# Performance work log

Hardware: AMD Instinct MI355X
Metric: run time of the kernel (lower is better)

The kernel has to match this reference:

```python
import jax, jax.numpy as jnp
import numpy as np

T, B, E, H = 2048, 2, 1024, 16
S = E // H


def setup_inputs() -> dict:
    key = jax.random.key(0)
    ks = jax.random.split(key, 7)
    sc = 1.0 / np.sqrt(S)
    return {
        "x": jax.random.normal(ks[0], (T, B, E), dtype=jnp.float32),
        "Wq": jax.random.normal(ks[1], (H, S, S), dtype=jnp.float32) * sc,
        "Wk": jax.random.normal(ks[2], (H, S, S), dtype=jnp.float32) * sc,
        "Wv": jax.random.normal(ks[3], (H, S, S), dtype=jnp.float32) * sc,
        "Er": jax.random.normal(ks[4], (S, T), dtype=jnp.float32),
        "Wr": jax.random.normal(ks[5], (E, E), dtype=jnp.float32) * (1.0 / np.sqrt(E)),
        "br": jax.random.normal(ks[6], (E,), dtype=jnp.float32) * 0.01,
    }


def reference(x, Wq, Wk, Wv, Er, Wr, br):
    # x: [t, b, e] -> [b, t, h, s]
    t, b, e = x.shape
    h = Wq.shape[0]
    s = e // h
    xh = jnp.transpose(x, (1, 0, 2)).reshape(b, t, h, s)
    # per-head no-bias linears (nn.Linear: y = x @ W.T), stacked over heads
    q = jnp.einsum('bths,hds->bhtd', xh, Wq)  # [b,h,t,s]
    k = jnp.einsum('bths,hds->bhtd', xh, Wk)
    v = jnp.einsum('bths,hds->bhtd', xh, Wv)
    # relative bias uses UNSCALED queries (computed before the 1/e^(1/4) scaling)
    srel = jnp.einsum('bhtd,dr->bhtr', q, Er)  # [b,h,t,t] since r == t
    scale = e ** 0.25
    scores = jnp.einsum('bhtd,bhrd->bhtr', q / scale, k / scale) + srel
    causal = jnp.triu(jnp.ones((t, t), dtype=bool), 1)
    scores = jnp.where(causal[None, None], jnp.float32(-1e9), scores)
    probs = jax.nn.softmax(scores, axis=-1)  # dropout is identity in eval
    out = jnp.einsum('bhtr,bhrd->bhtd', probs, v)  # [b,h,t,s]
    # torch.cat(heads, dim=2) == move head axis next to s
    out = jnp.transpose(out, (0, 2, 1, 3)).reshape(b, t, h * s)  # [b,t,e]
    # faithful to source quirk: transpose(1,2).contiguous().view(b,t,e)
    out = jnp.swapaxes(out, 1, 2).reshape(b, t, h * s)
    return out @ Wr.T + br
```

## Files before the change

kernel.cpp:

```cpp
#include <hip/hip_runtime.h>
#include <hip/hip_bf16.h>
#include <cstdio>

#define T_DIM 2048
#define B_DIM 2
#define E_DIM 1024
#define H_DIM 16
#define S_DIM 64
#define LOG2E 1.44269504088896340736f

typedef __attribute__((ext_vector_type(4))) float f32x4;
typedef __attribute__((ext_vector_type(16))) float f32x16;
typedef __attribute__((ext_vector_type(8))) short bf16x8;
typedef __attribute__((ext_vector_type(8))) unsigned short u16x8;
typedef __attribute__((ext_vector_type(4))) unsigned short u16x4;

#define MFMA32(a,b,c) __builtin_amdgcn_mfma_f32_32x32x16_bf16((a),(b),(c),0,0,0)

__device__ __forceinline__ unsigned short f2bf(float f) {
    union { __hip_bfloat16 h; unsigned short u; } c;
    c.h = __float2bfloat16(f);
    return c.u;
}
__device__ __forceinline__ void gload16(const void* g, void* l) {
    __builtin_amdgcn_global_load_lds(
        (const __attribute__((address_space(1))) unsigned int*)g,
        (__attribute__((address_space(3))) unsigned int*)l, 16, 0, 0);
}
__device__ __forceinline__ f32x16 zero16() {
    f32x16 v;
#pragma unroll
    for (int i = 0; i < 16; ++i) v[i] = 0.f;
    return v;
}

__global__ __launch_bounds__(256) void prep_w(
    const float* __restrict__ Wq, const float* __restrict__ Wk,
    const float* __restrict__ Wv, const float* __restrict__ Wr,
    unsigned short* __restrict__ whb, unsigned short* __restrict__ wrb)
{
    int bid = blockIdx.x;
    if (bid < 192) {
        int i = bid * 256 + threadIdx.x;
        const float* src = (i < 16384) ? Wq : ((i < 32768) ? Wk : Wv);
        float4 v = reinterpret_cast<const float4*>(src)[i & 16383];
        u16x4 o;
        o[0] = f2bf(v.x); o[1] = f2bf(v.y); o[2] = f2bf(v.z); o[3] = f2bf(v.w);
        *reinterpret_cast<u16x4*>(whb + (size_t)i * 4) = o;
    } else {
        int i = (bid - 192) * 256 + threadIdx.x;
        float4 v = reinterpret_cast<const float4*>(Wr)[i];
        u16x4 o;
        o[0] = f2bf(v.x); o[1] = f2bf(v.y); o[2] = f2bf(v.z); o[3] = f2bf(v.w);
        *reinterpret_cast<u16x4*>(wrb + (size_t)i * 4) = o;
    }
}

__global__ __launch_bounds__(64) void qkv_mfma(
    const float* __restrict__ x, const unsigned short* __restrict__ wb,
    const float* __restrict__ Er,
    unsigned short* __restrict__ qb_g, unsigned short* __restrict__ kh_g,
    unsigned short* __restrict__ vT_g)
{
    int bid = blockIdx.x;
    int dg = bid & 1;
    int tt = (bid >> 1) & 63;
    int h  = (bid >> 7) & 15;
    int b  = bid >> 11;
    int bh = b * H_DIM + h;
    int t0 = tt * 32;
    int lane = threadIdx.x;
    int l31 = lane & 31, hs = lane >> 5;

    bf16x8 xb[4];
    const float* xrow = x + (size_t)(t0 + l31) * (B_DIM * E_DIM) + (size_t)b * E_DIM + h * 64;
#pragma unroll
    for (int ks = 0; ks < 4; ++ks) {
        float vv[8];
        *reinterpret_cast<float4*>(&vv[0]) = *reinterpret_cast<const float4*>(xrow + ks * 16 + hs * 8);
        *reinterpret_cast<float4*>(&vv[4]) = *reinterpret_cast<const float4*>(xrow + ks * 16 + hs * 8 + 4);
        unsigned short hh[8];
#pragma unroll
        for (int j = 0; j < 8; ++j) hh[j] = f2bf(vv[j]);
        xb[ks] = *reinterpret_cast<bf16x8*>(hh);
    }

    f32x16 aq = zero16(), ak = zero16(), av = zero16();
    size_t wofs = (size_t)h * 4096 + (size_t)(dg * 32 + l31) * 64 + hs * 8;
#pragma unroll
    for (int ks = 0; ks < 4; ++ks) {
        bf16x8 qw = *reinterpret_cast<const bf16x8*>(wb + wofs + ks * 16);
        bf16x8 kw = *reinterpret_cast<const bf16x8*>(wb + 65536 + wofs + ks * 16);
        bf16x8 vw = *reinterpret_cast<const bf16x8*>(wb + 131072 + wofs + ks * 16);
        aq = MFMA32(xb[ks], qw, aq);
        ak = MFMA32(xb[ks], kw, ak);
        av = MFMA32(vw, xb[ks], av);
    }

    size_t rowbase = (size_t)bh * T_DIM * 64;
#pragma unroll
    for (int r = 0; r < 16; ++r) {
        int rowp = (r & 3) + 8 * (r >> 2) + 4 * hs;
        int t = t0 + rowp;
        int d = dg * 32 + l31;
        size_t ro = rowbase + (size_t)t * 64 + d;
        qb_g[ro] = f2bf(aq[r]);
        float kv = (ak[r] * 0.03125f + Er[(size_t)d * T_DIM + t]) * LOG2E;
        kh_g[ro] = f2bf(kv);
        vT_g[((size_t)bh * 64 + dg * 32 + rowp) * T_DIM + t0 + l31] = f2bf(av[r]);
    }
}

__global__ __launch_bounds__(256, 4) void attn_mfma32(
    const unsigned short* __restrict__ qb_g, const unsigned short* __restrict__ kh_g,
    const unsigned short* __restrict__ vT_g, unsigned short* __restrict__ attT)
{
    __shared__ __align__(16) unsigned char smem[33024];
    float* OT  = (float*)smem;
    float* MRG = (float*)smem;
    float* ML  = (float*)(smem + 32768);

    int bid = blockIdx.x;
    int bh = bid & 31;
    int u = bid >> 5;
    int j = u & 7, quad = u >> 3;
    int qt = (quad == 0) ? (31 - j) : (quad == 1) ? j
           : (quad == 2) ? (23 - j) : (8 + j);

    int tid = threadIdx.x;
    int w = tid >> 6;
    int half = w >> 1;
    int wq = w & 1;
    int lane = tid & 63;
    int l31 = lane & 31, hs = lane >> 5;
    int srow = lane >> 3, scol = lane & 7;
    int q_lo = qt * 64 + wq * 32;
    size_t base = (size_t)bh * T_DIM * 64;

    bf16x8 qB[4];
    {
        size_t qoff = base + (size_t)(q_lo + l31) * 64 + hs * 8;
#pragma unroll
        for (int st = 0; st < 4; ++st)
            qB[st] = *reinterpret_cast<const bf16x8*>(qb_g + qoff + st * 16);
    }

    f32x16 oacc0 = zero16(), oacc1 = zero16();
    float lsum = 0.f;

    unsigned char* KH = smem + half * 16384;
    unsigned char* VT = KH + 8192;

    int ntiles = qt + 1;
    int nst = (ntiles + 1) >> 1;

    for (int i = 0; i < nst; ++i) {
        int k0 = (2 * i + half) * 64;
        bool valid = k0 < ntiles * 64;
        __syncthreads();
        if (valid) {
#pragma unroll
            for (int ci = 0; ci < 4; ++ci) {
                int chunk = wq * 4 + ci;
                int row = chunk * 8 + srow;
                gload16(kh_g + base + (size_t)(k0 + row) * 64 + (scol ^ (row & 7)) * 8,
                        KH + chunk * 1024 + lane * 16);
            }
#pragma unroll
            for (int ci = 0; ci < 4; ++ci) {
                int chunk = wq * 4 + ci;
                int d = chunk * 8 + srow;
                gload16(vT_g + base + (size_t)d * T_DIM + k0 + ((scol ^ (d & 7)) * 8),
                        VT + chunk * 1024 + lane * 16);
            }
        }
        __syncthreads();
        if (valid) {
#pragma unroll
            for (int kt = 0; kt < 2; ++kt) {
                int ks = k0 + kt * 32;
                if (ks > q_lo) continue;
                int krow = kt * 32 + l31;
                f32x16 s = zero16();
                __builtin_amdgcn_s_setprio(1);
#pragma unroll
                for (int st = 0; st < 4; ++st) {
                    int slot = (st * 2 + hs) ^ (krow & 7);
                    bf16x8 kf = *reinterpret_cast<const bf16x8*>(KH + krow * 128 + slot * 16);
                    s = MFMA32(kf, qB[st], s);
                }
                __builtin_amdgcn_s_setprio(0);
                if (ks == q_lo) {
#pragma unroll
                    for (int r = 0; r < 16; ++r) {
                        int rowp = (r & 3) + 8 * (r >> 2) + 4 * hs;
                        if (rowp > l31) s[r] = -1e30f;
                    }
                }
                float p[16], psum = 0.f;
#pragma unroll
                for (int r = 0; r < 16; ++r) {
                    p[r] = __builtin_amdgcn_exp2f(s[r]);
                    psum += p[r];
                }
                lsum += psum + __shfl_xor(psum, 32);
                unsigned int wp[8];
#pragma unroll
                for (int q2 = 0; q2 < 2; ++q2) {
                    int o = q2 * 8, d2 = q2 * 4;
                    asm("v_cvt_pk_bf16_f32 %0, %1, %2" : "=v"(wp[d2+0]) : "v"(p[o+0]), "v"(p[o+1]));
                    asm("v_cvt_pk_bf16_f32 %0, %1, %2" : "=v"(wp[d2+1]) : "v"(p[o+2]), "v"(p[o+3]));
                    asm("v_cvt_pk_bf16_f32 %0, %1, %2" : "=v"(wp[d2+2]) : "v"(p[o+4]), "v"(p[o+5]));
                    asm("v_cvt_pk_bf16_f32 %0, %1, %2" : "=v"(wp[d2+3]) : "v"(p[o+6]), "v"(p[o+7]));
                    asm("v_permlane32_swap_b32 %0, %1" : "+v"(wp[d2+0]), "+v"(wp[d2+2]));
                    asm("v_permlane32_swap_b32 %0, %1" : "+v"(wp[d2+1]), "+v"(wp[d2+3]));
                }
                union { unsigned int u[4]; bf16x8 v; } pa0, pa1;
                pa0.u[0] = wp[0]; pa0.u[1] = wp[1]; pa0.u[2] = wp[2]; pa0.u[3] = wp[3];
                pa1.u[0] = wp[4]; pa1.u[1] = wp[5]; pa1.u[2] = wp[6]; pa1.u[3] = wp[7];
                __builtin_amdgcn_s_setprio(1);
#pragma unroll
                for (int ph = 0; ph < 2; ++ph) {
                    const bf16x8 pv = ph ? pa1.v : pa0.v;
#pragma unroll
                    for (int dt = 0; dt < 2; ++dt) {
                        int d = dt * 32 + l31;
                        int c = kt * 4 + ph * 2 + hs;
                        int slot = c ^ (d & 7);
                        bf16x8 vb = *reinterpret_cast<const bf16x8*>(VT + d * 128 + slot * 16);
                        if (dt == 0) oacc0 = MFMA32(vb, pv, oacc0);
                        else         oacc1 = MFMA32(vb, pv, oacc1);
                    }
                }
                __builtin_amdgcn_s_setprio(0);
            }
        }
    }

    __syncthreads();
    if (half == 1) {
#pragma unroll
        for (int r = 0; r < 16; ++r) {
            MRG[(wq * 32 + r) * 64 + lane]      = oacc0[r];
            MRG[(wq * 32 + 16 + r) * 64 + lane] = oacc1[r];
        }
        if (hs == 0) ML[wq * 32 + l31] = lsum;
    }
    __syncthreads();
    float inv = 0.f;
    if (half == 0) {
        lsum += ML[wq * 32 + l31];
        inv = 1.f / lsum;
#pragma unroll
        for (int r = 0; r < 16; ++r) {
            oacc0[r] += MRG[(wq * 32 + r) * 64 + lane];
            oacc1[r] += MRG[(wq * 32 + 16 + r) * 64 + lane];
        }
    }
    __syncthreads();

    if (half == 0) {
#pragma unroll
        for (int r = 0; r < 16; ++r) {
            int rowp = (r & 3) + 8 * (r >> 2) + 4 * hs;
            OT[(rowp)      * 68 + wq * 32 + l31] = oacc0[r] * inv;
            OT[(32 + rowp) * 68 + wq * 32 + l31] = oacc1[r] * inv;
        }
    }
    __syncthreads();
    {
        int d = tid >> 2, qb = tid & 3;
        unsigned short tmp[16];
#pragma unroll
        for (int i = 0; i < 4; ++i) {
            f32x4 v = *reinterpret_cast<const f32x4*>(&OT[d * 68 + qb * 16 + i * 4]);
            tmp[i*4+0] = f2bf(v[0]); tmp[i*4+1] = f2bf(v[1]);
            tmp[i*4+2] = f2bf(v[2]); tmp[i*4+3] = f2bf(v[3]);
        }
        unsigned short* dst = attT + ((size_t)bh * 64 + d) * T_DIM + qt * 64 + qb * 16;
        *reinterpret_cast<u16x8*>(dst)     = *reinterpret_cast<u16x8*>(&tmp[0]);
        *reinterpret_cast<u16x8*>(dst + 8) = *reinterpret_cast<u16x8*>(&tmp[8]);
    }
}

__global__ __launch_bounds__(256) void final_gemm_mfma(
    const unsigned short* __restrict__ A, const unsigned short* __restrict__ Bw,
    const float* __restrict__ br, float* __restrict__ out)
{
    __shared__ __align__(16) unsigned char gsm[49152];
    int nt = blockIdx.x;
    int mt = blockIdx.y;
    int tid = threadIdx.x;
    int w = tid >> 6;
    int lane = tid & 63;
    int l31 = lane & 31, hs = lane >> 5;
    int srow = lane >> 3, scol = lane & 7;

    auto stage = [&](int bs, int kt) {
        unsigned char* As = gsm + bs * 24576;
        unsigned char* Bs = As + 16384;
#pragma unroll
        for (int i = 0; i < 4; ++i) {
            int row = i * 32 + w * 8 + srow;
            gload16(A + (size_t)(mt * 128 + row) * 1024 + kt * 64 + ((scol ^ (row & 7)) * 8),
                    As + i * 4096 + w * 1024 + lane * 16);
        }
#pragma unroll
        for (int i = 0; i < 2; ++i) {
            int row = i * 32 + w * 8 + srow;
            gload16(Bw + (size_t)(nt * 64 + row) * 1024 + kt * 64 + ((scol ^ (row & 7)) * 8),
                    Bs + i * 4096 + w * 1024 + lane * 16);
        }
    };

    f32x16 oa0 = zero16(), oa1 = zero16();
    stage(0, 0);
    __syncthreads();
    for (int kt = 0; kt < 16; ++kt) {
        if (kt < 15) stage((kt + 1) & 1, kt + 1);
        const unsigned char* As = gsm + (kt & 1) * 24576;
        const unsigned char* Bs = As + 16384;
        int arow = w * 32 + l31;
        __builtin_amdgcn_s_setprio(1);
#pragma unroll
        for (int st = 0; st < 4; ++st) {
            int c = st * 2 + hs;
            bf16x8 af = *reinterpret_cast<const bf16x8*>(As + arow * 128 + ((c ^ (arow & 7)) * 16));
            {
                bf16x8 bf0 = *reinterpret_cast<const bf16x8*>(Bs + l31 * 128 + ((c ^ (l31 & 7)) * 16));
                oa0 = MFMA32(af, bf0, oa0);
            }
            {
                int brow = 32 + l31;
                bf16x8 bf1 = *reinterpret_cast<const bf16x8*>(Bs + brow * 128 + ((c ^ (brow & 7)) * 16));
                oa1 = MFMA32(af, bf1, oa1);
            }
        }
        __builtin_amdgcn_s_setprio(0);
        __syncthreads();
    }

#pragma unroll
    for (int ng = 0; ng < 2; ++ng) {
        int col = nt * 64 + ng * 32 + l31;
        float bias = br[col];
        const f32x16& oa = ng ? oa1 : oa0;
#pragma unroll
        for (int r = 0; r < 16; ++r) {
            int rowp = (r & 3) + 8 * (r >> 2) + 4 * hs;
            int row = mt * 128 + w * 32 + rowp;
            out[(size_t)row * 1024 + col] = oa[r] + bias;
        }
    }
}

extern "C" void kernel_launch(void* const* d_in, const int* in_sizes, int n_in,
                              void* d_out, int out_size, void* d_ws, size_t ws_size,
                              hipStream_t stream) {
    const float* x  = (const float*)d_in[0];
    const float* Wq = (const float*)d_in[1];
    const float* Wk = (const float*)d_in[2];
    const float* Wv = (const float*)d_in[3];
    const float* Er = (const float*)d_in[4];
    const float* Wr = (const float*)d_in[5];
    const float* br = (const float*)d_in[6];
    float* out = (float*)d_out;

    const size_t nQ = (size_t)B_DIM * H_DIM * T_DIM * S_DIM;
    char* p = (char*)d_ws;
    unsigned short* qb = (unsigned short*)p;   p += nQ * 2;
    unsigned short* kh = (unsigned short*)p;   p += nQ * 2;
    unsigned short* vT = (unsigned short*)p;   p += nQ * 2;
    unsigned short* attT = (unsigned short*)p; p += nQ * 2;
    unsigned short* wrb = (unsigned short*)p;  p += (size_t)E_DIM * E_DIM * 2;
    unsigned short* whb = (unsigned short*)p;  p += (size_t)3 * 65536 * 2;
    size_t need = (size_t)(p - (char*)d_ws);
    if (ws_size < need) {
        fprintf(stderr, "WS TOO SMALL: have %zu need %zu\n", ws_size, need);
        return;
    }

    prep_w<<<1216, 256, 0, stream>>>(Wq, Wk, Wv, Wr, whb, wrb);
    qkv_mfma<<<4096, 64, 0, stream>>>(x, whb, Er, qb, kh, vT);
    attn_mfma32<<<1024, 256, 0, stream>>>(qb, kh, vT, attT);
    final_gemm_mfma<<<dim3(16, 32), 256, 0, stream>>>(attT, wrb, br, out);
}
```

Measured before the change: 74.24 us.

## Change LDS XOR swizzle to avoid bank conflicts and interleave QK before softmax-PV

The LDS swizzle for the K, V^T and GEMM operand tiles now also XORs in the row-group bits, so 128-bit reads across a 32-row MFMA fragment spread over more banks. In the attention loop, both QK^T score tiles are computed before either softmax/PV step. This is meant to overlap MFMA latency with the exp and convert work. The cost is extra live registers for the second score tile, which could hurt occupancy.

```diff
diff --git a/kernel.cpp b/kernel.cpp
--- a/kernel.cpp
+++ b/kernel.cpp
@@ -134,6 +134,7 @@
     int lane = tid & 63;
     int l31 = lane & 31, hs = lane >> 5;
     int srow = lane >> 3, scol = lane & 7;
+    int lsw = (l31 & 7) ^ (((l31 >> 3) & 3) << 1);
     int q_lo = qt * 64 + wq * 32;
     size_t base = (size_t)bh * T_DIM * 64;
 
@@ -150,6 +151,65 @@
 
     unsigned char* KH = smem + half * 16384;
     unsigned char* VT = KH + 8192;
+
+    auto qk = [&](int kt) -> f32x16 {
+        int krow = kt * 32 + l31;
+        f32x16 s = zero16();
+        __builtin_amdgcn_s_setprio(1);
+#pragma unroll
+        for (int st = 0; st < 4; ++st) {
+            int slot = (st * 2 + hs) ^ lsw;
+            bf16x8 kf = *reinterpret_cast<const bf16x8*>(KH + krow * 128 + slot * 16);
+            s = MFMA32(kf, qB[st], s);
+        }
+        __builtin_amdgcn_s_setprio(0);
+        return s;
+    };
+
+    auto smpv = [&](f32x16& s, int kt, bool diag) {
+        if (diag) {
+#pragma unroll
+            for (int r = 0; r < 16; ++r) {
+                int rowp = (r & 3) + 8 * (r >> 2) + 4 * hs;
+                if (rowp > l31) s[r] = -1e30f;
+            }
+        }
+        float p[16], psum = 0.f;
+#pragma unroll
+        for (int r = 0; r < 16; ++r) {
+            p[r] = __builtin_amdgcn_exp2f(s[r]);
+            psum += p[r];
+        }
+        lsum += psum + __shfl_xor(psum, 32);
+        unsigned int wp[8];
+#pragma unroll
+        for (int q2 = 0; q2 < 2; ++q2) {
+            int o = q2 * 8, d2 = q2 * 4;
+            asm("v_cvt_pk_bf16_f32 %0, %1, %2" : "=v"(wp[d2+0]) : "v"(p[o+0]), "v"(p[o+1]));
+            asm("v_cvt_pk_bf16_f32 %0, %1, %2" : "=v"(wp[d2+1]) : "v"(p[o+2]), "v"(p[o+3]));
+            asm("v_cvt_pk_bf16_f32 %0, %1, %2" : "=v"(wp[d2+2]) : "v"(p[o+4]), "v"(p[o+5]));
+            asm("v_cvt_pk_bf16_f32 %0, %1, %2" : "=v"(wp[d2+3]) : "v"(p[o+6]), "v"(p[o+7]));
+            asm("v_permlane32_swap_b32 %0, %1" : "+v"(wp[d2+0]), "+v"(wp[d2+2]));
+            asm("v_permlane32_swap_b32 %0, %1" : "+v"(wp[d2+1]), "+v"(wp[d2+3]));
+        }
+        union { unsigned int u[4]; bf16x8 v; } pa0, pa1;
+        pa0.u[0] = wp[0]; pa0.u[1] = wp[1]; pa0.u[2] = wp[2]; pa0.u[3] = wp[3];
+        pa1.u[0] = wp[4]; pa1.u[1] = wp[5]; pa1.u[2] = wp[6]; pa1.u[3] = wp[7];
+        __builtin_amdgcn_s_setprio(1);
+#pragma unroll
+        for (int ph = 0; ph < 2; ++ph) {
+            const bf16x8 pv = ph ? pa1.v : pa0.v;
+#pragma unroll
+            for (int dt = 0; dt < 2; ++dt) {
+                int c = kt * 4 + ph * 2 + hs;
+                int slot = c ^ lsw;
+                bf16x8 vb = *reinterpret_cast<const bf16x8*>(VT + (dt * 32 + l31) * 128 + slot * 16);
+                if (dt == 0) oacc0 = MFMA32(vb, pv, oacc0);
+                else         oacc1 = MFMA32(vb, pv, oacc1);
+            }
+        }
+        __builtin_amdgcn_s_setprio(0);
+    };
 
     int ntiles = qt + 1;
     int nst = (ntiles + 1) >> 1;
@@ -163,76 +223,29 @@
             for (int ci = 0; ci < 4; ++ci) {
                 int chunk = wq * 4 + ci;
                 int row = chunk * 8 + srow;
-                gload16(kh_g + base + (size_t)(k0 + row) * 64 + (scol ^ (row & 7)) * 8,
+                int cd = scol ^ srow ^ ((ci & 3) << 1);
+                gload16(kh_g + base + (size_t)(k0 + row) * 64 + cd * 8,
                         KH + chunk * 1024 + lane * 16);
             }
 #pragma unroll
             for (int ci = 0; ci < 4; ++ci) {
                 int chunk = wq * 4 + ci;
                 int d = chunk * 8 + srow;
-                gload16(vT_g + base + (size_t)d * T_DIM + k0 + ((scol ^ (d & 7)) * 8),
+                int cd = scol ^ srow ^ ((ci & 3) << 1);
+                gload16(vT_g + base + (size_t)d * T_DIM + k0 + cd * 8,
                         VT + chunk * 1024 + lane * 16);
             }
         }
         __syncthreads();
         if (valid) {
-#pragma unroll
-            for (int kt = 0; kt < 2; ++kt) {
-                int ks = k0 + kt * 32;
-                if (ks > q_lo) continue;
-                int krow = kt * 32 + l31;
-                f32x16 s = zero16();
-                __builtin_amdgcn_s_setprio(1);
-#pragma unroll
-                for (int st = 0; st < 4; ++st) {
-                    int slot = (st * 2 + hs) ^ (krow & 7);
-                    bf16x8 kf = *reinterpret_cast<const bf16x8*>(KH + krow * 128 + slot * 16);
-                    s = MFMA32(kf, qB[st], s);
-                }
-                __builtin_amdgcn_s_setprio(0);
-                if (ks == q_lo) {
-#pragma unroll
-                    for (int r = 0; r < 16; ++r) {
-                        int rowp = (r & 3) + 8 * (r >> 2) + 4 * hs;
-                        if (rowp > l31) s[r] = -1e30f;
-                    }
-                }
-                float p[16], psum = 0.f;
-#pragma unroll
-                for (int r = 0; r < 16; ++r) {
-                    p[r] = __builtin_amdgcn_exp2f(s[r]);
-                    psum += p[r];
-                }
-                lsum += psum + __shfl_xor(psum, 32);
-                unsigned int wp[8];
-#pragma unroll
-                for (int q2 = 0; q2 < 2; ++q2) {
-                    int o = q2 * 8, d2 = q2 * 4;
-                    asm("v_cvt_pk_bf16_f32 %0, %1, %2" : "=v"(wp[d2+0]) : "v"(p[o+0]), "v"(p[o+1]));
-                    asm("v_cvt_pk_bf16_f32 %0, %1, %2" : "=v"(wp[d2+1]) : "v"(p[o+2]), "v"(p[o+3]));
-                    asm("v_cvt_pk_bf16_f32 %0, %1, %2" : "=v"(wp[d2+2]) : "v"(p[o+4]), "v"(p[o+5]));
-                    asm("v_cvt_pk_bf16_f32 %0, %1, %2" : "=v"(wp[d2+3]) : "v"(p[o+6]), "v"(p[o+7]));
-                    asm("v_permlane32_swap_b32 %0, %1" : "+v"(wp[d2+0]), "+v"(wp[d2+2]));
-                    asm("v_permlane32_swap_b32 %0, %1" : "+v"(wp[d2+1]), "+v"(wp[d2+3]));
-                }
-                union { unsigned int u[4]; bf16x8 v; } pa0, pa1;
-                pa0.u[0] = wp[0]; pa0.u[1] = wp[1]; pa0.u[2] = wp[2]; pa0.u[3] = wp[3];
-                pa1.u[0] = wp[4]; pa1.u[1] = wp[5]; pa1.u[2] = wp[6]; pa1.u[3] = wp[7];
-                __builtin_amdgcn_s_setprio(1);
-#pragma unroll
-                for (int ph = 0; ph < 2; ++ph) {
-                    const bf16x8 pv = ph ? pa1.v : pa0.v;
-#pragma unroll
-                    for (int dt = 0; dt < 2; ++dt) {
-                        int d = dt * 32 + l31;
-                        int c = kt * 4 + ph * 2 + hs;
-                        int slot = c ^ (d & 7);
-                        bf16x8 vb = *reinterpret_cast<const bf16x8*>(VT + d * 128 + slot * 16);
-                        if (dt == 0) oacc0 = MFMA32(vb, pv, oacc0);
-                        else         oacc1 = MFMA32(vb, pv, oacc1);
-                    }
-                }
-                __builtin_amdgcn_s_setprio(0);
+            bool two = (k0 + 32 <= q_lo);
+            f32x16 s0 = qk(0);
+            if (two) {
+                f32x16 s1 = qk(1);
+                smpv(s0, 0, false);
+                smpv(s1, 1, k0 + 32 == q_lo);
+            } else {
+                smpv(s0, 0, k0 == q_lo);
             }
         }
     }
@@ -295,6 +308,7 @@
     int lane = tid & 63;
     int l31 = lane & 31, hs = lane >> 5;
     int srow = lane >> 3, scol = lane & 7;
+    int lsw = (l31 & 7) ^ (((l31 >> 3) & 3) << 1);
 
     auto stage = [&](int bs, int kt) {
         unsigned char* As = gsm + bs * 24576;
@@ -302,13 +316,15 @@
 #pragma unroll
         for (int i = 0; i < 4; ++i) {
             int row = i * 32 + w * 8 + srow;
-            gload16(A + (size_t)(mt * 128 + row) * 1024 + kt * 64 + ((scol ^ (row & 7)) * 8),
+            int cd = scol ^ srow ^ (((row >> 3) & 3) << 1);
+            gload16(A + (size_t)(mt * 128 + row) * 1024 + kt * 64 + cd * 8,
                     As + i * 4096 + w * 1024 + lane * 16);
         }
 #pragma unroll
         for (int i = 0; i < 2; ++i) {
             int row = i * 32 + w * 8 + srow;
-            gload16(Bw + (size_t)(nt * 64 + row) * 1024 + kt * 64 + ((scol ^ (row & 7)) * 8),
+            int cd = scol ^ srow ^ (((row >> 3) & 3) << 1);
+            gload16(Bw + (size_t)(nt * 64 + row) * 1024 + kt * 64 + cd * 8,
                     Bs + i * 4096 + w * 1024 + lane * 16);
         }
     };
@@ -321,18 +337,19 @@
         const unsigned char* As = gsm + (kt & 1) * 24576;
         const unsigned char* Bs = As + 16384;
         int arow = w * 32 + l31;
+        int asw = (arow & 7) ^ (((arow >> 3) & 3) << 1);
         __builtin_amdgcn_s_setprio(1);
 #pragma unroll
         for (int st = 0; st < 4; ++st) {
             int c = st * 2 + hs;
-            bf16x8 af = *reinterpret_cast<const bf16x8*>(As + arow * 128 + ((c ^ (arow & 7)) * 16));
+            bf16x8 af = *reinterpret_cast<const bf16x8*>(As + arow * 128 + ((c ^ asw) * 16));
             {
-                bf16x8 bf0 = *reinterpret_cast<const bf16x8*>(Bs + l31 * 128 + ((c ^ (l31 & 7)) * 16));
+                bf16x8 bf0 = *reinterpret_cast<const bf16x8*>(Bs + l31 * 128 + ((c ^ lsw) * 16));
                 oa0 = MFMA32(af, bf0, oa0);
             }
             {
                 int brow = 32 + l31;
-                bf16x8 bf1 = *reinterpret_cast<const bf16x8*>(Bs + brow * 128 + ((c ^ (brow & 7)) * 16));
+                bf16x8 bf1 = *reinterpret_cast<const bf16x8*>(Bs + brow * 128 + ((c ^ lsw) * 16));
                 oa1 = MFMA32(af, bf1, oa1);
             }
         }
```

Measured after the change: 73.62 us. About the same (-0.8%).
